# Kernel tuning notes

Measured on AMD Instinct MI355X. Metric: run time of the kernel, lower is better.

Reference implementation:

```python
import jax, jax.numpy as jnp
import numpy as np

HID = 128   # Config.hidden_dim
K = 16      # kNN neighbors in TempEdgeConv
BIG = 1e9


def _glu(x, wl, bl, wg, bg):
    return (x @ wl + bl) * jax.nn.sigmoid(x @ wg + bg)


def _temp_edge_conv(h, t, w, b, k):
    # h: [G,n,d] node features, t: [G,n,1] temporal key feature
    # dynamic kNN graph on temporal distance within each graph
    d = jnp.abs(t - jnp.swapaxes(t, 1, 2))                  # [G,n,n]
    n = h.shape[1]
    d = d + jnp.eye(n, dtype=h.dtype) * BIG                  # exclude self
    _, idx = jax.lax.top_k(-d, k)                            # [G,n,k]
    hj = jax.vmap(lambda hg, ig: hg[ig])(h, idx)             # [G,n,k,d] gather
    hi = jnp.broadcast_to(h[:, :, None, :], hj.shape)
    e = jnp.concatenate([hi, hj - hi], axis=-1)              # [G,n,k,2d]
    e = e @ w + b                                            # edge MLP
    return jnp.max(e, axis=2)                                # max aggregation


def setup_inputs():
    key = jax.random.key(0)
    ks = jax.random.split(key, 18)
    G, n, IN, H = 64, 1024, 17, HID
    N = G * n
    feat = IN - 1                  # 16
    temb = H // 4                  # 32

    def lin(k1, i, o):
        ka, kb = jax.random.split(k1)
        return (jax.random.normal(ka, (i, o), jnp.float32) / np.sqrt(i),
                jax.random.normal(kb, (o,), jnp.float32) * 0.01)

    x = jax.random.normal(ks[0], (N, IN), jnp.float32)
    batch = jnp.repeat(jnp.arange(G, dtype=jnp.int32), n)
    te_w, te_b = lin(ks[1], 1, temb)
    ig_lw, ig_lb = lin(ks[2], feat + temb, H)
    ig_gw, ig_gb = lin(ks[3], feat + temb, H)
    c1_w, c1_b = lin(ks[4], 2 * H, H)
    c2_w, c2_b = lin(ks[5], 2 * H, H)
    fg_lw, fg_lb = lin(ks[6], 4 * H, H)
    fg_gw, fg_gb = lin(ks[7], 4 * H, H)
    out_w, out_b = lin(ks[8], H, 2)
    return {"x": x, "te_w": te_w, "te_b": te_b,
            "ig_lw": ig_lw, "ig_lb": ig_lb, "ig_gw": ig_gw, "ig_gb": ig_gb,
            "c1_w": c1_w, "c1_b": c1_b, "c2_w": c2_w, "c2_b": c2_b,
            "fg_lw": fg_lw, "fg_lb": fg_lb, "fg_gw": fg_gw, "fg_gb": fg_gb,
            "out_w": out_w, "out_b": out_b,
            "batch": batch, "num_graphs": 64}


def reference(x, te_w, te_b, ig_lw, ig_lb, ig_gw, ig_gb,
              c1_w, c1_b, c2_w, c2_b, fg_lw, fg_lb, fg_gw, fg_gb,
              out_w, out_b, batch, num_graphs):
    G = int(num_graphs)
    N = x.shape[0]
    n = N // G   # equal-sized graphs (batch = repeat(arange(G), n))
    key_feat = x[:, :1]                       # key_feature_idx == 0
    feats = x[:, 1:]
    t_emb = key_feat @ te_w + te_b            # time encoder [N, H//4]
    h = _glu(jnp.concatenate([feats, t_emb], axis=-1),
             ig_lw, ig_lb, ig_gw, ig_gb)      # [N, H] (dropout = identity, eval)
    h = h.reshape(G, n, HID)
    t = key_feat.reshape(G, n, 1)
    x1 = jax.nn.relu(_temp_edge_conv(h, t, c1_w, c1_b, K))   # [G,n,H]
    x2 = jax.nn.relu(_temp_edge_conv(x1, t, c2_w, c2_b, K))  # [G,n,H]
    comb = jnp.concatenate([x1, x2], axis=-1)                # [G,n,2H]
    pooled = jnp.concatenate([comb.max(axis=1), comb.mean(axis=1)], axis=-1)  # [G,4H]
    logits = _glu(pooled, fg_lw, fg_lb, fg_gw, fg_gb) @ out_w + out_b
    return jax.nn.log_softmax(logits, axis=-1)
```

## Files before the change

kernel.cpp:

```cpp
#include <hip/hip_runtime.h>
#include <math.h>

#define NN 65536
#define NG 64
#define NPG 1024
#define HID 128
#define KNN 16
#define BINF 1e30f

typedef unsigned long long ull;
typedef _Float16 f16;
typedef _Float16 f16x2 __attribute__((ext_vector_type(2)));
typedef _Float16 f16x8 __attribute__((ext_vector_type(8)));
typedef float f32x4 __attribute__((ext_vector_type(4)));

__global__ __launch_bounds__(256) void k_prep(
    const float* __restrict__ ig_lw, const float* __restrict__ ig_gw,
    const float* __restrict__ c1_w, const float* __restrict__ c2_w,
    f16* __restrict__ gfrag, f16* __restrict__ f1, f16* __restrict__ f2) {
    int gid = blockIdx.x * 256 + threadIdx.x;
    if (gid < 16384) {
        int i = gid & 7, lane = (gid >> 3) & 63, nt = (gid >> 9) & 7;
        int kt = (gid >> 12) & 1, mat = gid >> 13;
        int k = kt * 32 + ((lane >> 4) << 3) + i;
        int c = nt * 16 + (lane & 15);
        float v = 0.0f;
        if (k < 48) v = (mat ? ig_gw : ig_lw)[k * 128 + c];
        gfrag[gid] = (f16)v;
    } else {
        int g2 = gid - 16384;
        int buf = g2 >> 15;
        int rem = g2 & 32767;
        int mat = rem >> 14;
        int r2 = rem & 16383;
        int i = r2 & 7, lane = (r2 >> 3) & 63, nt = (r2 >> 9) & 7, kt = (r2 >> 12) & 3;
        int k = kt * 32 + ((lane >> 4) << 3) + i;
        int c = nt * 16 + (lane & 15);
        const float* cw = buf ? c2_w : c1_w;
        float top = cw[k * 128 + c];
        float bot = cw[(128 + k) * 128 + c];
        float v = mat ? bot : (top - bot);
        (buf ? f2 : f1)[rem] = (f16)v;
    }
}

__global__ __launch_bounds__(1024) void k_topk(const float* __restrict__ x,
                                               int* __restrict__ sidxg,
                                               signed char* __restrict__ nbroff) {
    __shared__ ull key[1024];
    __shared__ float st[1024];
    __shared__ int sidx[1024];
    int i = threadIdx.x;
    int g = blockIdx.x;
    float t = x[(size_t)(g * NPG + i) * 17];
    unsigned ub = __float_as_uint(t);
    ub = (ub & 0x80000000u) ? ~ub : (ub | 0x80000000u);
    key[i] = ((ull)ub << 32) | (unsigned)i;

    for (int k = 2; k <= 1024; k <<= 1) {
        for (int j = k >> 1; j > 0; j >>= 1) {
            __syncthreads();
            int ixj = i ^ j;
            if (ixj > i) {
                ull a = key[i], b = key[ixj];
                bool up = ((i & k) == 0);
                if ((a > b) == up) { key[i] = b; key[ixj] = a; }
            }
        }
    }
    __syncthreads();
    int oi = (int)(key[i] & 0xffffffffu);
    st[i] = x[(size_t)(g * NPG + oi) * 17];
    sidx[i] = oi;
    sidxg[g * NPG + i] = g * NPG + oi;
    __syncthreads();

    float tt = st[i];
    int L = i - 1, R = i + 1;
    signed char* out = nbroff + (size_t)(g * NPG + i) * KNN;
#pragma unroll
    for (int q = 0; q < KNN; q++) {
        float dl = (L >= 0)   ? (tt - st[L]) : BINF;
        float dr = (R < NPG) ? (st[R] - tt) : BINF;
        bool left;
        if (dl < dr) left = true;
        else if (dr < dl) left = false;
        else left = (sidx[L] < sidx[R]);
        int jr;
        if (left) { jr = L; L--; }
        else      { jr = R; R++; }
        out[q] = (signed char)(jr - i);
    }
}

__global__ __launch_bounds__(256) void k_glum(
    const float* __restrict__ x, const float* __restrict__ te_w,
    const float* __restrict__ te_b, const f16x8* __restrict__ wfrag,
    const float* __restrict__ bl, const float* __restrict__ bg,
    const int* __restrict__ sidxg, f16* __restrict__ H) {
    __shared__ f16x8 XL[4 * 2 * 64];
    int tid = threadIdx.x;
    int r0 = blockIdx.x * 64;
#pragma unroll
    for (int p = 0; p < 2; p++) {
        int idx = tid + p * 256;
        int row = idx >> 3, kq = idx & 7;
        int node = sidxg[r0 + row];
        f16x8 h;
        if (kq < 2) {
            const float* xr = x + (size_t)node * 17 + 1 + kq * 8;
#pragma unroll
            for (int i = 0; i < 8; i++) h[i] = (f16)xr[i];
        } else if (kq < 6) {
            float t = x[(size_t)node * 17];
            int j0 = (kq - 2) * 8;
#pragma unroll
            for (int i = 0; i < 8; i++) h[i] = (f16)fmaf(t, te_w[j0 + i], te_b[j0 + i]);
        } else {
#pragma unroll
            for (int i = 0; i < 8; i++) h[i] = (f16)0.0f;
        }
        int mf = row >> 4, kt = kq >> 2, lane = ((kq & 3) << 4) | (row & 15);
        XL[(mf * 2 + kt) * 64 + lane] = h;
    }
    __syncthreads();
    int w = tid >> 6, lane = tid & 63;
    f32x4 acc[2][2][4];
#pragma unroll
    for (int o = 0; o < 2; o++)
#pragma unroll
        for (int j = 0; j < 2; j++)
#pragma unroll
            for (int mf = 0; mf < 4; mf++) acc[o][j][mf] = (f32x4){0.f, 0.f, 0.f, 0.f};
#pragma unroll 1
    for (int kt = 0; kt < 2; kt++) {
        f16x8 wf0[2], wf1[2], xa[4];
#pragma unroll
        for (int j = 0; j < 2; j++) {
            wf0[j] = wfrag[((0 * 2 + kt) * 8 + (w * 2 + j)) * 64 + lane];
            wf1[j] = wfrag[((1 * 2 + kt) * 8 + (w * 2 + j)) * 64 + lane];
        }
#pragma unroll
        for (int mf = 0; mf < 4; mf++) xa[mf] = XL[(mf * 2 + kt) * 64 + lane];
#pragma unroll
        for (int mf = 0; mf < 4; mf++)
#pragma unroll
            for (int j = 0; j < 2; j++) {
                acc[0][j][mf] = __builtin_amdgcn_mfma_f32_16x16x32_f16(xa[mf], wf0[j], acc[0][j][mf], 0, 0, 0);
                acc[1][j][mf] = __builtin_amdgcn_mfma_f32_16x16x32_f16(xa[mf], wf1[j], acc[1][j][mf], 0, 0, 0);
            }
    }
#pragma unroll
    for (int j = 0; j < 2; j++) {
        int col = w * 32 + j * 16 + (lane & 15);
        float bbl = bl[col], bbg = bg[col];
#pragma unroll
        for (int mf = 0; mf < 4; mf++) {
            int rbase = r0 + mf * 16 + ((lane >> 4) << 2);
#pragma unroll
            for (int q = 0; q < 4; q++) {
                float lin = acc[0][j][mf][q] + bbl;
                float gat = acc[1][j][mf][q] + bbg;
                H[(size_t)(rbase + q) * 128 + col] = (f16)(lin / (1.0f + expf(-gat)));
            }
        }
    }
}

__global__ __launch_bounds__(256) void k_dualm(
    const f16* __restrict__ H, const f16x8* __restrict__ wfrag,
    const float* __restrict__ cb, f16* __restrict__ A, f16* __restrict__ B) {
    __shared__ f16x8 XL[4 * 4 * 64];
    int tid = threadIdx.x;
    int r0 = blockIdx.x * 64;
#pragma unroll
    for (int p = 0; p < 4; p++) {
        int idx = tid + p * 256;
        int row = idx >> 4, kq = idx & 15;
        f16x8 h = *(const f16x8*)(H + (size_t)(r0 + row) * 128 + kq * 8);
        int mf = row >> 4, kt = kq >> 2, lane = ((kq & 3) << 4) | (row & 15);
        XL[(mf * 4 + kt) * 64 + lane] = h;
    }
    __syncthreads();
    int w = tid >> 6, lane = tid & 63;
    f32x4 acc[2][2][4];
#pragma unroll
    for (int o = 0; o < 2; o++)
#pragma unroll
        for (int j = 0; j < 2; j++)
#pragma unroll
            for (int mf = 0; mf < 4; mf++) acc[o][j][mf] = (f32x4){0.f, 0.f, 0.f, 0.f};
#pragma unroll 1
    for (int kt = 0; kt < 4; kt++) {
        f16x8 wf0[2], wf1[2], xa[4];
#pragma unroll
        for (int j = 0; j < 2; j++) {
            wf0[j] = wfrag[((0 * 4 + kt) * 8 + (w * 2 + j)) * 64 + lane];
            wf1[j] = wfrag[((1 * 4 + kt) * 8 + (w * 2 + j)) * 64 + lane];
        }
#pragma unroll
        for (int mf = 0; mf < 4; mf++) xa[mf] = XL[(mf * 4 + kt) * 64 + lane];
#pragma unroll
        for (int mf = 0; mf < 4; mf++)
#pragma unroll
            for (int j = 0; j < 2; j++) {
                acc[0][j][mf] = __builtin_amdgcn_mfma_f32_16x16x32_f16(xa[mf], wf0[j], acc[0][j][mf], 0, 0, 0);
                acc[1][j][mf] = __builtin_amdgcn_mfma_f32_16x16x32_f16(xa[mf], wf1[j], acc[1][j][mf], 0, 0, 0);
            }
    }
#pragma unroll
    for (int j = 0; j < 2; j++) {
        int col = w * 32 + j * 16 + (lane & 15);
        float bias = cb[col];
#pragma unroll
        for (int mf = 0; mf < 4; mf++) {
            int rbase = r0 + mf * 16 + ((lane >> 4) << 2);
#pragma unroll
            for (int q = 0; q < 4; q++) {
                A[(size_t)(rbase + q) * 128 + col] = (f16)(acc[0][j][mf][q] + bias);
                B[(size_t)(rbase + q) * 128 + col] = (f16)acc[1][j][mf][q];
            }
        }
    }
}

__global__ __launch_bounds__(256) void k_conv2f(
    const f16* __restrict__ A1, const f16* __restrict__ B1,
    const signed char* __restrict__ nbroff, const f16x8* __restrict__ wfrag,
    const float* __restrict__ cb, f16* __restrict__ x1,
    f16* __restrict__ A2, f16* __restrict__ B2) {
    __shared__ f16 Bwin[96 * 128];
    __shared__ f16 x1t[64 * 128];
    int tid = threadIdx.x;
    int bx = blockIdx.x;
    int r0 = bx * 64;
    int r0loc = (bx & 15) * 64;
#pragma unroll
    for (int p = 0; p < 6; p++) {
        int idx = tid + p * 256;
        int row = idx >> 4, kq = idx & 15;
        int gl = r0loc - 16 + row;
        f16x8 v;
#pragma unroll
        for (int i = 0; i < 8; i++) v[i] = (f16)0.0f;
        if (gl >= 0 && gl < NPG)
            v = *(const f16x8*)(B1 + (size_t)(r0 - 16 + row) * 128 + kq * 8);
        *(f16x8*)&Bwin[row * 128 + kq * 8] = v;
    }
    __syncthreads();
    int w = tid >> 6, lane = tid & 63;
    int c0 = lane * 2;
    for (int rr = 0; rr < 16; rr++) {
        int row = w * 16 + rr;
        int grow = r0 + row;
        int4 ov = *(const int4*)(nbroff + (size_t)grow * 16);
        const int* ow = (const int*)&ov;
        f16x2 av = *(const f16x2*)(A1 + (size_t)grow * 128 + c0);
        float m0 = -BINF, m1 = -BINF;
#pragma unroll
        for (int q = 0; q < 16; q++) {
            int off = (int)(signed char)((ow[q >> 2] >> ((q & 3) * 8)) & 0xff);
            f16x2 bv = *(const f16x2*)&Bwin[(row + 16 + off) * 128 + c0];
            m0 = fmaxf(m0, (float)bv[0]);
            m1 = fmaxf(m1, (float)bv[1]);
        }
        float v0 = fmaxf((float)av[0] + m0, 0.0f);
        float v1 = fmaxf((float)av[1] + m1, 0.0f);
        f16x2 xv; xv[0] = (f16)v0; xv[1] = (f16)v1;
        *(f16x2*)&x1t[(row * 128 + c0) ^ ((row & 7) << 3)] = xv;
        *(f16x2*)(x1 + (size_t)grow * 128 + c0) = xv;
    }
    __syncthreads();
    f32x4 acc[2][2][4];
#pragma unroll
    for (int o = 0; o < 2; o++)
#pragma unroll
        for (int j = 0; j < 2; j++)
#pragma unroll
            for (int mf = 0; mf < 4; mf++) acc[o][j][mf] = (f32x4){0.f, 0.f, 0.f, 0.f};
    int row16 = lane & 15, kslot = lane >> 4;
    int swz = (row16 & 7) << 3;
#pragma unroll 1
    for (int kt = 0; kt < 4; kt++) {
        f16x8 wf0[2], wf1[2], xa[4];
#pragma unroll
        for (int j = 0; j < 2; j++) {
            wf0[j] = wfrag[((0 * 4 + kt) * 8 + (w * 2 + j)) * 64 + lane];
            wf1[j] = wfrag[((1 * 4 + kt) * 8 + (w * 2 + j)) * 64 + lane];
        }
#pragma unroll
        for (int mf = 0; mf < 4; mf++)
            xa[mf] = *(const f16x8*)&x1t[((mf * 16 + row16) * 128 + kt * 32 + kslot * 8) ^ swz];
#pragma unroll
        for (int mf = 0; mf < 4; mf++)
#pragma unroll
            for (int j = 0; j < 2; j++) {
                acc[0][j][mf] = __builtin_amdgcn_mfma_f32_16x16x32_f16(xa[mf], wf0[j], acc[0][j][mf], 0, 0, 0);
                acc[1][j][mf] = __builtin_amdgcn_mfma_f32_16x16x32_f16(xa[mf], wf1[j], acc[1][j][mf], 0, 0, 0);
            }
    }
#pragma unroll
    for (int j = 0; j < 2; j++) {
        int col = w * 32 + j * 16 + (lane & 15);
        float bias = cb[col];
#pragma unroll
        for (int mf = 0; mf < 4; mf++) {
            int rbase = r0 + mf * 16 + ((lane >> 4) << 2);
#pragma unroll
            for (int q = 0; q < 4; q++) {
                A2[(size_t)(rbase + q) * 128 + col] = (f16)(acc[0][j][mf][q] + bias);
                B2[(size_t)(rbase + q) * 128 + col] = (f16)acc[1][j][mf][q];
            }
        }
    }
}

__global__ __launch_bounds__(256) void k_gather2p(
    const f16* __restrict__ A2, const f16* __restrict__ B2,
    const f16* __restrict__ x1, const signed char* __restrict__ nbroff,
    float* __restrict__ partM, float* __restrict__ partS) {
    __shared__ f16 Bwin[96 * 128];
    __shared__ float red[4 * 64 * 8];
    int tid = threadIdx.x;
    int bx = blockIdx.x;
    int r0 = bx * 64;
    int r0loc = (bx & 15) * 64;
#pragma unroll
    for (int p = 0; p < 6; p++) {
        int idx = tid + p * 256;
        int row = idx >> 4, kq = idx & 15;
        int gl = r0loc - 16 + row;
        f16x8 v;
#pragma unroll
        for (int i = 0; i < 8; i++) v[i] = (f16)0.0f;
        if (gl >= 0 && gl < NPG)
            v = *(const f16x8*)(B2 + (size_t)(r0 - 16 + row) * 128 + kq * 8);
        *(f16x8*)&Bwin[row * 128 + kq * 8] = v;
    }
    __syncthreads();
    int w = tid >> 6, lane = tid & 63;
    int c0 = lane * 2;
    float m1a = -BINF, m1b = -BINF, s1a = 0.f, s1b = 0.f;
    float m2a = -BINF, m2b = -BINF, s2a = 0.f, s2b = 0.f;
    for (int rr = 0; rr < 16; rr++) {
        int row = w * 16 + rr;
        int grow = r0 + row;
        int4 ov = *(const int4*)(nbroff + (size_t)grow * 16);
        const int* ow = (const int*)&ov;
        f16x2 av = *(const f16x2*)(A2 + (size_t)grow * 128 + c0);
        float m0 = -BINF, m1 = -BINF;
#pragma unroll
        for (int q = 0; q < 16; q++) {
            int off = (int)(signed char)((ow[q >> 2] >> ((q & 3) * 8)) & 0xff);
            f16x2 bv = *(const f16x2*)&Bwin[(row + 16 + off) * 128 + c0];
            m0 = fmaxf(m0, (float)bv[0]);
            m1 = fmaxf(m1, (float)bv[1]);
        }
        float v0 = fmaxf((float)av[0] + m0, 0.0f);
        float v1 = fmaxf((float)av[1] + m1, 0.0f);
        m2a = fmaxf(m2a, v0); s2a += v0;
        m2b = fmaxf(m2b, v1); s2b += v1;
        f16x2 xv = *(const f16x2*)(x1 + (size_t)grow * 128 + c0);
        float u0 = (float)xv[0], u1 = (float)xv[1];
        m1a = fmaxf(m1a, u0); s1a += u0;
        m1b = fmaxf(m1b, u1); s1b += u1;
    }
    int rb = (w * 64 + lane) * 8;
    red[rb + 0] = m1a; red[rb + 1] = s1a; red[rb + 2] = m2a; red[rb + 3] = s2a;
    red[rb + 4] = m1b; red[rb + 5] = s1b; red[rb + 6] = m2b; red[rb + 7] = s2b;
    __syncthreads();
    if (tid < 128) {
        int l2 = tid >> 1, j = tid & 1;
        float M1 = -BINF, S1 = 0.f, M2 = -BINF, S2 = 0.f;
#pragma unroll
        for (int w2 = 0; w2 < 4; w2++) {
            int b2 = (w2 * 64 + l2) * 8 + j * 4;
            M1 = fmaxf(M1, red[b2 + 0]); S1 += red[b2 + 1];
            M2 = fmaxf(M2, red[b2 + 2]); S2 += red[b2 + 3];
        }
        size_t ob = (size_t)bx * 256;
        partM[ob + tid] = M1;        partS[ob + tid] = S1;
        partM[ob + 128 + tid] = M2;  partS[ob + 128 + tid] = S2;
    }
}

__global__ __launch_bounds__(256) void k_final(const float* __restrict__ partM,
                                               const float* __restrict__ partS,
                                               const float* __restrict__ fg_lw,
                                               const float* __restrict__ fg_lb,
                                               const float* __restrict__ fg_gw,
                                               const float* __restrict__ fg_gb,
                                               const float* __restrict__ out_w,
                                               const float* __restrict__ out_b,
                                               float* __restrict__ out) {
    __shared__ float pooled[512];
    __shared__ float linv[128], gatev[128];
    __shared__ float gluv[128];
    __shared__ float lg[2];
    int g = blockIdx.x, tid = threadIdx.x;

    float mx = -BINF, sm = 0.0f;
    for (int ch = 0; ch < 16; ch++) {
        mx = fmaxf(mx, partM[(size_t)(g * 16 + ch) * 256 + tid]);
        sm += partS[(size_t)(g * 16 + ch) * 256 + tid];
    }
    pooled[tid] = mx;
    pooled[256 + tid] = sm * (1.0f / 1024.0f);
    __syncthreads();

    float acc = 0.0f;
    if (tid < 128) {
        for (int k = 0; k < 512; k++) acc = fmaf(pooled[k], fg_lw[k * 128 + tid], acc);
        linv[tid] = acc + fg_lb[tid];
    } else {
        int c = tid - 128;
        for (int k = 0; k < 512; k++) acc = fmaf(pooled[k], fg_gw[k * 128 + c], acc);
        gatev[c] = acc + fg_gb[c];
    }
    __syncthreads();
    if (tid < 128) gluv[tid] = linv[tid] / (1.0f + expf(-gatev[tid]));
    __syncthreads();
    if (tid < 2) {
        float s = out_b[tid];
        for (int c = 0; c < 128; c++) s = fmaf(gluv[c], out_w[c * 2 + tid], s);
        lg[tid] = s;
    }
    __syncthreads();
    if (tid < 2) {
        float m = fmaxf(lg[0], lg[1]);
        float lse = m + logf(expf(lg[0] - m) + expf(lg[1] - m));
        out[g * 2 + tid] = lg[tid] - lse;
    }
}

extern "C" void kernel_launch(void* const* d_in, const int* in_sizes, int n_in,
                              void* d_out, int out_size, void* d_ws, size_t ws_size,
                              hipStream_t stream) {
    const float* x     = (const float*)d_in[0];
    const float* te_w  = (const float*)d_in[1];
    const float* te_b  = (const float*)d_in[2];
    const float* ig_lw = (const float*)d_in[3];
    const float* ig_lb = (const float*)d_in[4];
    const float* ig_gw = (const float*)d_in[5];
    const float* ig_gb = (const float*)d_in[6];
    const float* c1_w  = (const float*)d_in[7];
    const float* c1_b  = (const float*)d_in[8];
    const float* c2_w  = (const float*)d_in[9];
    const float* c2_b  = (const float*)d_in[10];
    const float* fg_lw = (const float*)d_in[11];
    const float* fg_lb = (const float*)d_in[12];
    const float* fg_gw = (const float*)d_in[13];
    const float* fg_gb = (const float*)d_in[14];
    const float* out_w = (const float*)d_in[15];
    const float* out_b = (const float*)d_in[16];
    float* out = (float*)d_out;

    char* p = (char*)d_ws;
    const size_t T16 = (size_t)NN * HID * sizeof(f16);
    f16* H  = (f16*)p; p += T16;
    f16* A1 = (f16*)p; p += T16;
    f16* B1 = (f16*)p; p += T16;
    f16* x1 = (f16*)p; p += T16;
    f16* A2 = (f16*)p; p += T16;
    f16* B2 = (f16*)p; p += T16;
    int* sidxg = (int*)p;            p += (size_t)NN * 4;
    signed char* nbroff = (signed char*)p; p += (size_t)NN * KNN;
    float* partM = (float*)p;        p += (size_t)1024 * 256 * 4;
    float* partS = (float*)p;        p += (size_t)1024 * 256 * 4;
    f16* gfrag = (f16*)p;            p += 16384 * 2;
    f16* f1 = (f16*)p;               p += 32768 * 2;
    f16* f2 = (f16*)p;               p += 32768 * 2;

    k_prep<<<320, 256, 0, stream>>>(ig_lw, ig_gw, c1_w, c2_w, gfrag, f1, f2);
    k_topk<<<NG, 1024, 0, stream>>>(x, sidxg, nbroff);
    k_glum<<<NN / 64, 256, 0, stream>>>(x, te_w, te_b, (const f16x8*)gfrag,
                                        ig_lb, ig_gb, sidxg, H);
    k_dualm<<<NN / 64, 256, 0, stream>>>(H, (const f16x8*)f1, c1_b, A1, B1);
    k_conv2f<<<NN / 64, 256, 0, stream>>>(A1, B1, nbroff, (const f16x8*)f2,
                                          c2_b, x1, A2, B2);
    k_gather2p<<<NN / 64, 256, 0, stream>>>(A2, B2, x1, nbroff, partM, partS);
    k_final<<<NG, 256, 0, stream>>>(partM, partS, fg_lw, fg_lb, fg_gw, fg_gb,
                                    out_w, out_b, out);
}
```

Measured before the change: 127.1 us.

## Fuse input GLU with conv1 matmul, pool x1 in conv2, shuffle-based bitonic sort

Merges the input GLU kernel and the first dual-projection matmul into one kernel that keeps the hidden tile in swizzled shared memory, so the H tensor never goes through global memory. The x1 max/sum pooling moves into the conv2 kernel, which removes the x1 global write and its re-read in the final gather. The bitonic sort in top-k now keeps keys in registers and uses warp shuffles for strides below 64, cutting shared-memory traffic and barriers. The costs are more shared memory per block in the fused kernel and one extra partial-reduction buffer.

```diff
diff --git a/kernel.cpp b/kernel.cpp
--- a/kernel.cpp
+++ b/kernel.cpp
@@ -55,21 +55,27 @@
     float t = x[(size_t)(g * NPG + i) * 17];
     unsigned ub = __float_as_uint(t);
     ub = (ub & 0x80000000u) ? ~ub : (ub | 0x80000000u);
-    key[i] = ((ull)ub << 32) | (unsigned)i;
+    ull kk = ((ull)ub << 32) | (unsigned)i;
 
     for (int k = 2; k <= 1024; k <<= 1) {
         for (int j = k >> 1; j > 0; j >>= 1) {
-            __syncthreads();
-            int ixj = i ^ j;
-            if (ixj > i) {
-                ull a = key[i], b = key[ixj];
-                bool up = ((i & k) == 0);
-                if ((a > b) == up) { key[i] = b; key[ixj] = a; }
-            }
-        }
-    }
-    __syncthreads();
-    int oi = (int)(key[i] & 0xffffffffu);
+            ull pv;
+            if (j >= 64) {
+                key[i] = kk;
+                __syncthreads();
+                pv = key[i ^ j];
+                __syncthreads();
+            } else {
+                pv = __shfl_xor(kk, j, 64);
+            }
+            bool up = ((i & k) == 0);
+            bool low = ((i & j) == 0);
+            ull mn = kk < pv ? kk : pv;
+            ull mx = kk < pv ? pv : kk;
+            kk = (up == low) ? mn : mx;
+        }
+    }
+    int oi = (int)(kk & 0xffffffffu);
     st[i] = x[(size_t)(g * NPG + oi) * 17];
     sidx[i] = oi;
     sidxg[g * NPG + i] = g * NPG + oi;
@@ -93,12 +99,14 @@
     }
 }
 
-__global__ __launch_bounds__(256) void k_glum(
+__global__ __launch_bounds__(256) void k_fuse1(
     const float* __restrict__ x, const float* __restrict__ te_w,
-    const float* __restrict__ te_b, const f16x8* __restrict__ wfrag,
+    const float* __restrict__ te_b, const f16x8* __restrict__ gfrag,
     const float* __restrict__ bl, const float* __restrict__ bg,
-    const int* __restrict__ sidxg, f16* __restrict__ H) {
+    const int* __restrict__ sidxg, const f16x8* __restrict__ wfrag,
+    const float* __restrict__ cb, f16* __restrict__ A, f16* __restrict__ B) {
     __shared__ f16x8 XL[4 * 2 * 64];
+    __shared__ f16 ht[64 * 128];
     int tid = threadIdx.x;
     int r0 = blockIdx.x * 64;
 #pragma unroll
@@ -137,8 +145,8 @@
         f16x8 wf0[2], wf1[2], xa[4];
 #pragma unroll
         for (int j = 0; j < 2; j++) {
-            wf0[j] = wfrag[((0 * 2 + kt) * 8 + (w * 2 + j)) * 64 + lane];
-            wf1[j] = wfrag[((1 * 2 + kt) * 8 + (w * 2 + j)) * 64 + lane];
+            wf0[j] = gfrag[((0 * 2 + kt) * 8 + (w * 2 + j)) * 64 + lane];
+            wf1[j] = gfrag[((1 * 2 + kt) * 8 + (w * 2 + j)) * 64 + lane];
         }
 #pragma unroll
         for (int mf = 0; mf < 4; mf++) xa[mf] = XL[(mf * 2 + kt) * 64 + lane];
@@ -156,40 +164,25 @@
         float bbl = bl[col], bbg = bg[col];
 #pragma unroll
         for (int mf = 0; mf < 4; mf++) {
-            int rbase = r0 + mf * 16 + ((lane >> 4) << 2);
+            int rloc = mf * 16 + ((lane >> 4) << 2);
 #pragma unroll
             for (int q = 0; q < 4; q++) {
                 float lin = acc[0][j][mf][q] + bbl;
                 float gat = acc[1][j][mf][q] + bbg;
-                H[(size_t)(rbase + q) * 128 + col] = (f16)(lin / (1.0f + expf(-gat)));
-            }
-        }
-    }
-}
-
-__global__ __launch_bounds__(256) void k_dualm(
-    const f16* __restrict__ H, const f16x8* __restrict__ wfrag,
-    const float* __restrict__ cb, f16* __restrict__ A, f16* __restrict__ B) {
-    __shared__ f16x8 XL[4 * 4 * 64];
-    int tid = threadIdx.x;
-    int r0 = blockIdx.x * 64;
-#pragma unroll
-    for (int p = 0; p < 4; p++) {
-        int idx = tid + p * 256;
-        int row = idx >> 4, kq = idx & 15;
-        f16x8 h = *(const f16x8*)(H + (size_t)(r0 + row) * 128 + kq * 8);
-        int mf = row >> 4, kt = kq >> 2, lane = ((kq & 3) << 4) | (row & 15);
-        XL[(mf * 4 + kt) * 64 + lane] = h;
-    }
-    __syncthreads();
-    int w = tid >> 6, lane = tid & 63;
-    f32x4 acc[2][2][4];
+                int row = rloc + q;
+                ht[(row * 128 + col) ^ ((row & 7) << 3)] = (f16)(lin / (1.0f + expf(-gat)));
+            }
+        }
+    }
+    __syncthreads();
 #pragma unroll
     for (int o = 0; o < 2; o++)
 #pragma unroll
         for (int j = 0; j < 2; j++)
 #pragma unroll
             for (int mf = 0; mf < 4; mf++) acc[o][j][mf] = (f32x4){0.f, 0.f, 0.f, 0.f};
+    int row16 = lane & 15, kslot = lane >> 4;
+    int swz = (row16 & 7) << 3;
 #pragma unroll 1
     for (int kt = 0; kt < 4; kt++) {
         f16x8 wf0[2], wf1[2], xa[4];
@@ -199,7 +192,8 @@
             wf1[j] = wfrag[((1 * 4 + kt) * 8 + (w * 2 + j)) * 64 + lane];
         }
 #pragma unroll
-        for (int mf = 0; mf < 4; mf++) xa[mf] = XL[(mf * 4 + kt) * 64 + lane];
+        for (int mf = 0; mf < 4; mf++)
+            xa[mf] = *(const f16x8*)&ht[((mf * 16 + row16) * 128 + kt * 32 + kslot * 8) ^ swz];
 #pragma unroll
         for (int mf = 0; mf < 4; mf++)
 #pragma unroll
@@ -227,10 +221,12 @@
 __global__ __launch_bounds__(256) void k_conv2f(
     const f16* __restrict__ A1, const f16* __restrict__ B1,
     const signed char* __restrict__ nbroff, const f16x8* __restrict__ wfrag,
-    const float* __restrict__ cb, f16* __restrict__ x1,
-    f16* __restrict__ A2, f16* __restrict__ B2) {
+    const float* __restrict__ cb, f16* __restrict__ A2, f16* __restrict__ B2,
+    float* __restrict__ partM1, float* __restrict__ partS1) {
     __shared__ f16 Bwin[96 * 128];
     __shared__ f16 x1t[64 * 128];
+    __shared__ float redM[4 * 128];
+    __shared__ float redS[4 * 128];
     int tid = threadIdx.x;
     int bx = blockIdx.x;
     int r0 = bx * 64;
@@ -250,6 +246,7 @@
     __syncthreads();
     int w = tid >> 6, lane = tid & 63;
     int c0 = lane * 2;
+    float m1a = -BINF, m1b = -BINF, s1a = 0.f, s1b = 0.f;
     for (int rr = 0; rr < 16; rr++) {
         int row = w * 16 + rr;
         int grow = r0 + row;
@@ -266,11 +263,24 @@
         }
         float v0 = fmaxf((float)av[0] + m0, 0.0f);
         float v1 = fmaxf((float)av[1] + m1, 0.0f);
+        m1a = fmaxf(m1a, v0); s1a += v0;
+        m1b = fmaxf(m1b, v1); s1b += v1;
         f16x2 xv; xv[0] = (f16)v0; xv[1] = (f16)v1;
         *(f16x2*)&x1t[(row * 128 + c0) ^ ((row & 7) << 3)] = xv;
-        *(f16x2*)(x1 + (size_t)grow * 128 + c0) = xv;
-    }
-    __syncthreads();
+    }
+    redM[w * 128 + c0] = m1a; redM[w * 128 + c0 + 1] = m1b;
+    redS[w * 128 + c0] = s1a; redS[w * 128 + c0 + 1] = s1b;
+    __syncthreads();
+    if (tid < 128) {
+        float M = -BINF, S = 0.f;
+#pragma unroll
+        for (int w2 = 0; w2 < 4; w2++) {
+            M = fmaxf(M, redM[w2 * 128 + tid]);
+            S += redS[w2 * 128 + tid];
+        }
+        partM1[(size_t)bx * 128 + tid] = M;
+        partS1[(size_t)bx * 128 + tid] = S;
+    }
     f32x4 acc[2][2][4];
 #pragma unroll
     for (int o = 0; o < 2; o++)
@@ -317,10 +327,11 @@
 
 __global__ __launch_bounds__(256) void k_gather2p(
     const f16* __restrict__ A2, const f16* __restrict__ B2,
-    const f16* __restrict__ x1, const signed char* __restrict__ nbroff,
-    float* __restrict__ partM, float* __restrict__ partS) {
+    const signed char* __restrict__ nbroff,
+    float* __restrict__ partM2, float* __restrict__ partS2) {
     __shared__ f16 Bwin[96 * 128];
-    __shared__ float red[4 * 64 * 8];
+    __shared__ float redM[4 * 128];
+    __shared__ float redS[4 * 128];
     int tid = threadIdx.x;
     int bx = blockIdx.x;
     int r0 = bx * 64;
@@ -340,7 +351,6 @@
     __syncthreads();
     int w = tid >> 6, lane = tid & 63;
     int c0 = lane * 2;
-    float m1a = -BINF, m1b = -BINF, s1a = 0.f, s1b = 0.f;
     float m2a = -BINF, m2b = -BINF, s2a = 0.f, s2b = 0.f;
     for (int rr = 0; rr < 16; rr++) {
         int row = w * 16 + rr;
@@ -360,32 +370,26 @@
         float v1 = fmaxf((float)av[1] + m1, 0.0f);
         m2a = fmaxf(m2a, v0); s2a += v0;
         m2b = fmaxf(m2b, v1); s2b += v1;
-        f16x2 xv = *(const f16x2*)(x1 + (size_t)grow * 128 + c0);
-        float u0 = (float)xv[0], u1 = (float)xv[1];
-        m1a = fmaxf(m1a, u0); s1a += u0;
-        m1b = fmaxf(m1b, u1); s1b += u1;
-    }
-    int rb = (w * 64 + lane) * 8;
-    red[rb + 0] = m1a; red[rb + 1] = s1a; red[rb + 2] = m2a; red[rb + 3] = s2a;
-    red[rb + 4] = m1b; red[rb + 5] = s1b; red[rb + 6] = m2b; red[rb + 7] = s2b;
+    }
+    redM[w * 128 + c0] = m2a; redM[w * 128 + c0 + 1] = m2b;
+    redS[w * 128 + c0] = s2a; redS[w * 128 + c0 + 1] = s2b;
     __syncthreads();
     if (tid < 128) {
-        int l2 = tid >> 1, j = tid & 1;
-        float M1 = -BINF, S1 = 0.f, M2 = -BINF, S2 = 0.f;
+        float M = -BINF, S = 0.f;
 #pragma unroll
         for (int w2 = 0; w2 < 4; w2++) {
-            int b2 = (w2 * 64 + l2) * 8 + j * 4;
-            M1 = fmaxf(M1, red[b2 + 0]); S1 += red[b2 + 1];
-            M2 = fmaxf(M2, red[b2 + 2]); S2 += red[b2 + 3];
-        }
-        size_t ob = (size_t)bx * 256;
-        partM[ob + tid] = M1;        partS[ob + tid] = S1;
-        partM[ob + 128 + tid] = M2;  partS[ob + 128 + tid] = S2;
-    }
-}
-
-__global__ __launch_bounds__(256) void k_final(const float* __restrict__ partM,
-                                               const float* __restrict__ partS,
+            M = fmaxf(M, redM[w2 * 128 + tid]);
+            S += redS[w2 * 128 + tid];
+        }
+        partM2[(size_t)bx * 128 + tid] = M;
+        partS2[(size_t)bx * 128 + tid] = S;
+    }
+}
+
+__global__ __launch_bounds__(256) void k_final(const float* __restrict__ partM1,
+                                               const float* __restrict__ partS1,
+                                               const float* __restrict__ partM2,
+                                               const float* __restrict__ partS2,
                                                const float* __restrict__ fg_lw,
                                                const float* __restrict__ fg_lb,
                                                const float* __restrict__ fg_gw,
@@ -399,10 +403,13 @@
     __shared__ float lg[2];
     int g = blockIdx.x, tid = threadIdx.x;
 
+    const float* pM = (tid < 128) ? partM1 : partM2;
+    const float* pS = (tid < 128) ? partS1 : partS2;
+    int cc = tid & 127;
     float mx = -BINF, sm = 0.0f;
     for (int ch = 0; ch < 16; ch++) {
-        mx = fmaxf(mx, partM[(size_t)(g * 16 + ch) * 256 + tid]);
-        sm += partS[(size_t)(g * 16 + ch) * 256 + tid];
+        mx = fmaxf(mx, pM[(size_t)(g * 16 + ch) * 128 + cc]);
+        sm += pS[(size_t)(g * 16 + ch) * 128 + cc];
     }
     pooled[tid] = mx;
     pooled[256 + tid] = sm * (1.0f / 1024.0f);
@@ -457,28 +464,28 @@
 
     char* p = (char*)d_ws;
     const size_t T16 = (size_t)NN * HID * sizeof(f16);
-    f16* H  = (f16*)p; p += T16;
     f16* A1 = (f16*)p; p += T16;
     f16* B1 = (f16*)p; p += T16;
-    f16* x1 = (f16*)p; p += T16;
     f16* A2 = (f16*)p; p += T16;
     f16* B2 = (f16*)p; p += T16;
     int* sidxg = (int*)p;            p += (size_t)NN * 4;
     signed char* nbroff = (signed char*)p; p += (size_t)NN * KNN;
-    float* partM = (float*)p;        p += (size_t)1024 * 256 * 4;
-    float* partS = (float*)p;        p += (size_t)1024 * 256 * 4;
+    float* partM1 = (float*)p;       p += (size_t)1024 * 128 * 4;
+    float* partS1 = (float*)p;       p += (size_t)1024 * 128 * 4;
+    float* partM2 = (float*)p;       p += (size_t)1024 * 128 * 4;
+    float* partS2 = (float*)p;       p += (size_t)1024 * 128 * 4;
     f16* gfrag = (f16*)p;            p += 16384 * 2;
     f16* f1 = (f16*)p;               p += 32768 * 2;
     f16* f2 = (f16*)p;               p += 32768 * 2;
 
     k_prep<<<320, 256, 0, stream>>>(ig_lw, ig_gw, c1_w, c2_w, gfrag, f1, f2);
     k_topk<<<NG, 1024, 0, stream>>>(x, sidxg, nbroff);
-    k_glum<<<NN / 64, 256, 0, stream>>>(x, te_w, te_b, (const f16x8*)gfrag,
-                                        ig_lb, ig_gb, sidxg, H);
-    k_dualm<<<NN / 64, 256, 0, stream>>>(H, (const f16x8*)f1, c1_b, A1, B1);
+    k_fuse1<<<NN / 64, 256, 0, stream>>>(x, te_w, te_b, (const f16x8*)gfrag,
+                                         ig_lb, ig_gb, sidxg, (const f16x8*)f1,
+                                         c1_b, A1, B1);
     k_conv2f<<<NN / 64, 256, 0, stream>>>(A1, B1, nbroff, (const f16x8*)f2,
-                                          c2_b, x1, A2, B2);
-    k_gather2p<<<NN / 64, 256, 0, stream>>>(A2, B2, x1, nbroff, partM, partS);
-    k_final<<<NG, 256, 0, stream>>>(partM, partS, fg_lw, fg_lb, fg_gw, fg_gb,
-                                    out_w, out_b, out);
-}
+                                          c2_b, A2, B2, partM1, partS1);
+    k_gather2p<<<NN / 64, 256, 0, stream>>>(A2, B2, nbroff, partM2, partS2);
+    k_final<<<NG, 256, 0, stream>>>(partM1, partS1, partM2, partS2,
+                                    fg_lw, fg_lb, fg_gw, fg_gb, out_w, out_b, out);
+}
```

Result: faster. 120.1 us (-5.5%).
